# Kernel optimization log

Hardware: AMD Instinct MI355X
Metric: run time of the kernel (lower is better)

## Reference

```python
import math
import jax, jax.numpy as jnp
import numpy as np

D_EMBD = 1024
N_HEAD = 16
BLOCK = 2048
B, T = 4, 2048


def setup_inputs() -> dict:
    key = jax.random.key(0)
    ks = jax.random.split(key, 5)
    d = D_EMBD
    return {
        "x": jax.random.normal(ks[0], (B, T, d), dtype=jnp.float32),
        "Wq": jax.random.normal(ks[1], (d, d), dtype=jnp.float32),
        "bq": jnp.zeros((d,), dtype=jnp.float32),
        "Wk": jax.random.normal(ks[2], (d, d), dtype=jnp.float32),
        "bk": jnp.zeros((d,), dtype=jnp.float32),
        "Wv": jax.random.normal(ks[3], (d, d), dtype=jnp.float32),
        "bv": jnp.zeros((d,), dtype=jnp.float32),
        "Wp": jax.random.normal(ks[4], (d, d), dtype=jnp.float32),
        "bp": jnp.zeros((d,), dtype=jnp.float32),
    }


def reference(x, Wq, bq, Wk, bk, Wv, bv, Wp, bp):
    Bb, Tt, C = x.shape
    n_head = N_HEAD
    hd = C // n_head  # head dim
    # QKV projections -> [B, H, T, hd]
    def split_heads(y):
        return y.reshape(Bb, Tt, n_head, hd).transpose(0, 2, 1, 3)
    Q = split_heads(x @ Wq + bq)
    K = split_heads(x @ Wk + bk)
    V = split_heads(x @ Wv + bv)
    # scores [B, H, T, T]
    attn = jnp.einsum('bhqd,bhkd->bhqk', Q, K) / math.sqrt(hd)
    # causal mask: -inf strictly above diagonal (matches triu(ones*-inf, 1))
    causal = jnp.tril(jnp.ones((Tt, Tt), dtype=bool))
    attn = jnp.where(causal, attn, -jnp.inf)
    attn = jax.nn.softmax(attn, axis=-1)
    y = jnp.einsum('bhqk,bhkd->bhqd', attn, V)
    y = y.transpose(0, 2, 1, 3).reshape(Bb, Tt, C)
    return y @ Wp + bp
```

## Files before the change

kernel.cpp:

```cpp
#include <hip/hip_runtime.h>
#include <stdint.h>
#include <stddef.h>

#define TT 2048
#define CC 1024
#define BBATCH 4
#define HH 16
#define HD 64
#define MTOT (BBATCH * TT)

typedef __bf16 bf16_t;
typedef __bf16 bf16x4 __attribute__((ext_vector_type(4)));
typedef __bf16 bf16x8 __attribute__((ext_vector_type(8)));
typedef float f32x4 __attribute__((ext_vector_type(4)));
typedef float f32x16 __attribute__((ext_vector_type(16)));

typedef const __attribute__((address_space(1))) uint32_t* as1_u32p;
typedef __attribute__((address_space(3))) uint32_t* as3_u32p;

__device__ __forceinline__ f32x4 mfma16(bf16x8 a, bf16x8 b, f32x4 c) {
  return __builtin_amdgcn_mfma_f32_16x16x32_bf16(a, b, c, 0, 0, 0);
}
__device__ __forceinline__ f32x16 mfma32(bf16x8 a, bf16x8 b, f32x16 c) {
  return __builtin_amdgcn_mfma_f32_32x32x16_bf16(a, b, c, 0, 0, 0);
}

__device__ __forceinline__ void gload_lds16(void* lds, const void* g) {
  __builtin_amdgcn_global_load_lds((as1_u32p)g, (as3_u32p)lds, 16, 0, 0);
}

__device__ __forceinline__ bf16x8 rd32(const char* t, int row, int lane) {
  int sl = (lane >> 4) ^ ((row >> 1) & 3);
  return *(const bf16x8*)(t + row * 64 + sl * 16);
}
__device__ __forceinline__ bf16x8 rd32r(const char* t, int row, int slot) {
  return *(const bf16x8*)(t + row * 128 + ((slot ^ (row & 7)) * 16));
}

__global__ void split_x_kernel(const float* __restrict__ x, bf16_t* __restrict__ xh,
                               bf16_t* __restrict__ xl, int n4) {
  int stride = gridDim.x * blockDim.x;
  for (int i = blockIdx.x * blockDim.x + threadIdx.x; i < n4; i += stride) {
    float4 v = ((const float4*)x)[i];
    float vv[4] = {v.x, v.y, v.z, v.w};
    bf16x4 hv, lv;
#pragma unroll
    for (int j = 0; j < 4; ++j) {
      bf16_t h = (bf16_t)vv[j];
      hv[j] = h;
      lv[j] = (bf16_t)(vv[j] - (float)h);
    }
    *(bf16x4*)(xh + (size_t)i * 4) = hv;
    *(bf16x4*)(xl + (size_t)i * 4) = lv;
  }
}

__global__ void transpose_split_kernel(const float* __restrict__ Wq, const float* __restrict__ Wk,
                                       const float* __restrict__ Wv, const float* __restrict__ Wp,
                                       bf16_t* __restrict__ wqkh, bf16_t* __restrict__ wqkl,
                                       bf16_t* __restrict__ wv_t, bf16_t* __restrict__ wp_t) {
  __shared__ float tile[32][33];
  int mat = blockIdx.z;
  const float* W = (mat == 0) ? Wq : (mat == 1) ? Wk : (mat == 2) ? Wv : Wp;
  int tx = threadIdx.x, ty = threadIdx.y;
  int n0 = blockIdx.x * 32, k0 = blockIdx.y * 32;
#pragma unroll
  for (int j = 0; j < 32; j += 8)
    tile[ty + j][tx] = W[(size_t)(k0 + ty + j) * CC + n0 + tx];
  __syncthreads();
#pragma unroll
  for (int j = 0; j < 32; j += 8) {
    float v = tile[tx][ty + j];
    int n = n0 + ty + j, k = k0 + tx;
    if (mat <= 1) {
      bf16_t h = (bf16_t)v;
      size_t o = (size_t)(mat * CC + n) * CC + k;
      wqkh[o] = h;
      wqkl[o] = (bf16_t)(v - (float)h);
    } else {
      bf16_t* dst = (mat == 2) ? wv_t : wp_t;
      dst[(size_t)n * CC + k] = (bf16_t)v;
    }
  }
}

__global__ __launch_bounds__(512, 2) void gemm_qk_kernel(
    const bf16_t* __restrict__ Ah, const bf16_t* __restrict__ Al,
    const bf16_t* __restrict__ Bh, const bf16_t* __restrict__ Bl,
    const float* __restrict__ bq, const float* __restrict__ bk,
    bf16_t* __restrict__ qh, bf16_t* __restrict__ ql,
    bf16_t* __restrict__ kh, bf16_t* __restrict__ kl) {
  __shared__ __align__(16) char s_ah[2][16384];
  __shared__ __align__(16) char s_al[2][16384];
  __shared__ __align__(16) char s_bh[2][16384];
  __shared__ __align__(16) char s_bl[2][16384];

  const int blk = blockIdx.x;
  const int bn = blk & 7;
  const int bm = blk >> 3;
  const int tid = threadIdx.x, w = tid >> 6, lane = tid & 63;
  const int wr = w >> 2, wc = w & 3;
  const int qi = lane & 15, hi = lane >> 4;

  const int c0 = w * 2, c1 = w * 2 + 1;
  const int srow0 = c0 * 16 + (lane >> 2);
  const int srow1 = c1 * 16 + (lane >> 2);
  const int ssl0 = (lane & 3) ^ ((srow0 >> 1) & 3);
  const int ssl1 = (lane & 3) ^ ((srow1 >> 1) & 3);
  const size_t a_off0 = (size_t)(bm * 256 + srow0) * CC + ssl0 * 8;
  const size_t a_off1 = (size_t)(bm * 256 + srow1) * CC + ssl1 * 8;
  const size_t b_off0 = (size_t)(bn * 256 + srow0) * CC + ssl0 * 8;
  const size_t b_off1 = (size_t)(bn * 256 + srow1) * CC + ssl1 * 8;

  f32x4 acc[8][4] = {};

#define STAGE_QK(buf, k0)                                        \
  do {                                                           \
    gload_lds16(s_ah[buf] + c0 * 1024, Ah + a_off0 + (k0));      \
    gload_lds16(s_ah[buf] + c1 * 1024, Ah + a_off1 + (k0));      \
    gload_lds16(s_al[buf] + c0 * 1024, Al + a_off0 + (k0));      \
    gload_lds16(s_al[buf] + c1 * 1024, Al + a_off1 + (k0));      \
    gload_lds16(s_bh[buf] + c0 * 1024, Bh + b_off0 + (k0));      \
    gload_lds16(s_bh[buf] + c1 * 1024, Bh + b_off1 + (k0));      \
    gload_lds16(s_bl[buf] + c0 * 1024, Bl + b_off0 + (k0));      \
    gload_lds16(s_bl[buf] + c1 * 1024, Bl + b_off1 + (k0));      \
  } while (0)

  STAGE_QK(0, 0);
  int cur = 0;
  for (int ks = 0; ks < 32; ++ks) {
    if (ks < 31) {
      STAGE_QK(cur ^ 1, (ks + 1) * 32);
      asm volatile("s_waitcnt vmcnt(8)" ::: "memory");
    } else {
      asm volatile("s_waitcnt vmcnt(0)" ::: "memory");
    }
    __builtin_amdgcn_s_barrier();

    bf16x8 bfh[4], bfl[4];
#pragma unroll
    for (int ni = 0; ni < 4; ++ni) {
      int br = wc * 64 + ni * 16 + qi;
      bfh[ni] = rd32(s_bh[cur], br, lane);
      bfl[ni] = rd32(s_bl[cur], br, lane);
    }
    __builtin_amdgcn_s_setprio(1);
#pragma unroll
    for (int mi = 0; mi < 8; ++mi) {
      int ar = wr * 128 + mi * 16 + qi;
      bf16x8 ahf = rd32(s_ah[cur], ar, lane);
      bf16x8 alf = rd32(s_al[cur], ar, lane);
#pragma unroll
      for (int ni = 0; ni < 4; ++ni) {
        acc[mi][ni] = mfma16(ahf, bfh[ni], acc[mi][ni]);
        acc[mi][ni] = mfma16(ahf, bfl[ni], acc[mi][ni]);
        acc[mi][ni] = mfma16(alf, bfh[ni], acc[mi][ni]);
      }
    }
    __builtin_amdgcn_s_setprio(0);
    asm volatile("s_waitcnt lgkmcnt(0)" ::: "memory");
    __builtin_amdgcn_s_barrier();
    cur ^= 1;
  }
#undef STAGE_QK

  const int which = bn >> 2;
  const float* bias = which ? bk : bq;
  bf16_t* oh = which ? kh : qh;
  bf16_t* ol = which ? kl : ql;
#pragma unroll
  for (int mi = 0; mi < 8; ++mi) {
#pragma unroll
    for (int ni = 0; ni < 4; ++ni) {
      const int col = bn * 256 + wc * 64 + ni * 16 + qi;
      const int c1i = col & 1023;
      const int h = c1i >> 6, d = c1i & 63;
#pragma unroll
      for (int r = 0; r < 4; ++r) {
        const int row = bm * 256 + wr * 128 + mi * 16 + hi * 4 + r;
        const int b = row >> 11, t = row & 2047;
        float v = acc[mi][ni][r] + bias[c1i];
        if (!which) v *= 0.125f;
        const size_t off = ((size_t)(b * HH + h) * TT + t) * HD + d;
        bf16_t hv = (bf16_t)v;
        oh[off] = hv;
        ol[off] = (bf16_t)(v - (float)hv);
      }
    }
  }
}

template <int MODE>
__global__ __launch_bounds__(256) void gemm_kernel(
    const bf16_t* __restrict__ Ah,
    const bf16_t* __restrict__ Bh,
    const float* __restrict__ bias0,
    void* __restrict__ out0) {
  __shared__ __align__(16) char smem[2 * 8192];
  char* sAh = smem;
  char* sBh = smem + 8192;

  const int bn = blockIdx.x, bm = blockIdx.y;
  const int tid = threadIdx.x, w = tid >> 6, lane = tid & 63;
  const int wr = w >> 1, wc = w & 1;

  f32x4 acc[4][4] = {};

  for (int ks = 0; ks < 32; ++ks) {
    const int k0 = ks * 32;
    __syncthreads();
#pragma unroll
    for (int it = 0; it < 2; ++it) {
      int c = it * 4 + w;
      int row = c * 16 + (lane >> 2);
      int sl = (lane & 3) ^ ((row >> 1) & 3);
      size_t aoff = (size_t)(bm * 128 + row) * CC + k0 + sl * 8;
      size_t boff = (size_t)(bn * 128 + row) * CC + k0 + sl * 8;
      gload_lds16(sAh + c * 1024, Ah + aoff);
      gload_lds16(sBh + c * 1024, Bh + boff);
    }
    __syncthreads();

    bf16x8 afh[4], bfh[4];
#pragma unroll
    for (int i = 0; i < 4; ++i) {
      int ar = wr * 64 + i * 16 + (lane & 15);
      int br = wc * 64 + i * 16 + (lane & 15);
      afh[i] = rd32(sAh, ar, lane);
      bfh[i] = rd32(sBh, br, lane);
    }
#pragma unroll
    for (int mi = 0; mi < 4; ++mi) {
#pragma unroll
      for (int ni = 0; ni < 4; ++ni) {
        acc[mi][ni] = mfma16(afh[mi], bfh[ni], acc[mi][ni]);
      }
    }
  }

#pragma unroll
  for (int mi = 0; mi < 4; ++mi) {
#pragma unroll
    for (int ni = 0; ni < 4; ++ni) {
      const int col = bn * 128 + wc * 64 + ni * 16 + (lane & 15);
#pragma unroll
      for (int r = 0; r < 4; ++r) {
        const int row = bm * 128 + wr * 64 + mi * 16 + (lane >> 4) * 4 + r;
        float v = acc[mi][ni][r];
        if (MODE == 1) {
          const int h = col >> 6, d = col & 63;
          const int b = row >> 11, t = row & 2047;
          float vv = v + bias0[col];
          ((bf16_t*)out0)[((size_t)(b * HH + h) * HD + d) * TT + t] = (bf16_t)vv;
        } else {
          ((float*)out0)[(size_t)row * CC + col] = v + bias0[col];
        }
      }
    }
  }
}

__global__ __launch_bounds__(512, 1) void attn_kernel(
    const bf16_t* __restrict__ qh, const bf16_t* __restrict__ ql,
    const bf16_t* __restrict__ kh, const bf16_t* __restrict__ kl,
    const bf16_t* __restrict__ vt, bf16_t* __restrict__ y) {
  __shared__ __align__(16) char s_kh[2][8192];
  __shared__ __align__(16) char s_kl[2][8192];
  __shared__ __align__(16) char s_vt[2][8192];

  const int blk = blockIdx.x;
  const int qb = (int)((0x12560347u >> ((blk >> 6) * 4)) & 7u);
  const int bh = (blk & 7) * 8 + ((blk >> 3) & 7);
  const int b = bh >> 4, h = bh & 15;
  const int tid = threadIdx.x, w = tid >> 6, lane = tid & 63;
  const int l31 = lane & 31, hi = lane >> 5;

  const int strow = w * 8 + (lane >> 3);
  const int sl = (lane & 7) ^ (strow & 7);
  const int ksrow = (strow & ~12) | ((strow & 4) << 1) | ((strow & 8) >> 1);
  const size_t koff = ((size_t)bh * TT + ksrow) * HD + sl * 8;
  const size_t voff = ((size_t)bh * HD + strow) * TT + sl * 8;
  const int ch = w * 1024;

#define STAGE_ATTN(buf, kt)                                            \
  do {                                                                 \
    gload_lds16(s_kh[buf] + ch, kh + koff + (size_t)(kt) * 64 * HD);   \
    gload_lds16(s_kl[buf] + ch, kl + koff + (size_t)(kt) * 64 * HD);   \
    gload_lds16(s_vt[buf] + ch, vt + voff + (size_t)(kt) * 64);        \
  } while (0)

  const int ktmax = 4 * qb + 3;
  const int qrow0 = qb * 256 + w * 32;
  const int qv = qrow0 + l31;

  bf16x8 qhf[4], qlf[4];
#pragma unroll
  for (int kc = 0; kc < 4; ++kc) {
    size_t off = ((size_t)bh * TT + qv) * HD + kc * 16 + hi * 8;
    qhf[kc] = *(const bf16x8*)(qh + off);
    qlf[kc] = *(const bf16x8*)(ql + off);
  }

  f32x16 o0 = {}, o1 = {};
  float m = -1e30f, l = 0.f;

  STAGE_ATTN(0, 0);
  int cur = 0;
  for (int kt = 0; kt <= ktmax; ++kt) {
    if (kt < ktmax) {
      STAGE_ATTN(cur ^ 1, kt + 1);
      asm volatile("s_waitcnt vmcnt(3)" ::: "memory");
    } else {
      asm volatile("s_waitcnt vmcnt(0)" ::: "memory");
    }
    __builtin_amdgcn_s_barrier();

    const char* ckh = s_kh[cur];
    const char* ckl = s_kl[cur];
    const char* cvt = s_vt[cur];
    const bool active = (qrow0 + 31 >= kt * 64);
    if (active) {
      f32x16 s0 = {}, s1 = {};
#pragma unroll
      for (int kc = 0; kc < 4; ++kc) {
        bf16x8 kfh = rd32r(ckh, l31, kc * 2 + hi);
        bf16x8 kfl = rd32r(ckl, l31, kc * 2 + hi);
        s0 = mfma32(kfh, qhf[kc], s0);
        s0 = mfma32(kfl, qhf[kc], s0);
        s0 = mfma32(kfh, qlf[kc], s0);
      }
#pragma unroll
      for (int kc = 0; kc < 4; ++kc) {
        bf16x8 kfh = rd32r(ckh, 32 + l31, kc * 2 + hi);
        bf16x8 kfl = rd32r(ckl, 32 + l31, kc * 2 + hi);
        s1 = mfma32(kfh, qhf[kc], s1);
        s1 = mfma32(kfl, qhf[kc], s1);
        s1 = mfma32(kfh, qlf[kc], s1);
      }

      if (kt * 64 + 63 > qrow0) {
#pragma unroll
        for (int r = 0; r < 16; ++r) {
          const int kvb = kt * 64 + (r & 7) + 8 * hi + 16 * (r >> 3);
          if (kvb > qv) s0[r] = -1e30f;
          if (kvb + 32 > qv) s1[r] = -1e30f;
        }
      }

      float t8[8];
#pragma unroll
      for (int r = 0; r < 8; ++r)
        t8[r] = fmaxf(fmaxf(s0[r], s0[r + 8]), fmaxf(s1[r], s1[r + 8]));
      float t4a = fmaxf(t8[0], t8[4]), t4b = fmaxf(t8[1], t8[5]);
      float t4c = fmaxf(t8[2], t8[6]), t4d = fmaxf(t8[3], t8[7]);
      float tmax = fmaxf(fmaxf(t4a, t4b), fmaxf(t4c, t4d));
      tmax = fmaxf(tmax, __shfl_xor(tmax, 32));

      const float mnew = fmaxf(m, tmax);
      if (!__all(tmax <= m)) {
        const float sc = __expf(m - mnew);
        l *= sc;
#pragma unroll
        for (int r = 0; r < 16; ++r) { o0[r] *= sc; o1[r] *= sc; }
        m = mnew;
      }

#pragma unroll
      for (int r = 0; r < 16; ++r) {
        s0[r] = __expf(s0[r] - m);
        s1[r] = __expf(s1[r] - m);
      }
      float p8[8];
#pragma unroll
      for (int r = 0; r < 8; ++r)
        p8[r] = (s0[r] + s0[r + 8]) + (s1[r] + s1[r + 8]);
      float ps = ((p8[0] + p8[1]) + (p8[2] + p8[3])) + ((p8[4] + p8[5]) + (p8[6] + p8[7]));
      ps += __shfl_xor(ps, 32);
      l += ps;

      bf16x8 pa[4];
#pragma unroll
      for (int cc = 0; cc < 4; ++cc) {
#pragma unroll
        for (int j = 0; j < 8; ++j)
          pa[cc][j] = (bf16_t)((cc >> 1) ? s1[8 * (cc & 1) + j] : s0[8 * (cc & 1) + j]);
      }

#pragma unroll
      for (int cc = 0; cc < 4; ++cc) {
        bf16x8 vf0 = rd32r(cvt, l31, cc * 2 + hi);
        bf16x8 vf1 = rd32r(cvt, 32 + l31, cc * 2 + hi);
        o0 = mfma32(vf0, pa[cc], o0);
        o1 = mfma32(vf1, pa[cc], o1);
      }
    }

    asm volatile("s_waitcnt lgkmcnt(0)" ::: "memory");
    __builtin_amdgcn_s_barrier();
    cur ^= 1;
  }

  const float inv = 1.f / l;
  bf16_t* yb = y + (size_t)(b * TT + qv) * CC + h * HD;
#pragma unroll
  for (int g = 0; g < 4; ++g) {
    bf16x4 ov0, ov1;
#pragma unroll
    for (int r = 0; r < 4; ++r) {
      ov0[r] = (bf16_t)(o0[g * 4 + r] * inv);
      ov1[r] = (bf16_t)(o1[g * 4 + r] * inv);
    }
    *(bf16x4*)(yb + g * 8 + hi * 4) = ov0;
    *(bf16x4*)(yb + 32 + g * 8 + hi * 4) = ov1;
  }
#undef STAGE_ATTN
}

extern "C" void kernel_launch(void* const* d_in, const int* in_sizes, int n_in,
                              void* d_out, int out_size, void* d_ws, size_t ws_size,
                              hipStream_t stream) {
  (void)in_sizes; (void)n_in; (void)out_size; (void)ws_size;
  const float* x  = (const float*)d_in[0];
  const float* Wq = (const float*)d_in[1];
  const float* bq = (const float*)d_in[2];
  const float* Wk = (const float*)d_in[3];
  const float* bk = (const float*)d_in[4];
  const float* Wv = (const float*)d_in[5];
  const float* bv = (const float*)d_in[6];
  const float* Wp = (const float*)d_in[7];
  const float* bp = (const float*)d_in[8];

  char* ws = (char*)d_ws;
  const size_t MB = 1024 * 1024;
  bf16_t* xh   = (bf16_t*)(ws + 0 * MB);
  bf16_t* xl   = (bf16_t*)(ws + 16 * MB);
  bf16_t* wqkh = (bf16_t*)(ws + 32 * MB);
  bf16_t* wqkl = (bf16_t*)(ws + 36 * MB);
  bf16_t* wv_t = (bf16_t*)(ws + 40 * MB);
  bf16_t* wp_t = (bf16_t*)(ws + 42 * MB);
  bf16_t* qhw  = (bf16_t*)(ws + 44 * MB);
  bf16_t* qlw  = (bf16_t*)(ws + 60 * MB);
  bf16_t* khw  = (bf16_t*)(ws + 76 * MB);
  bf16_t* klw  = (bf16_t*)(ws + 92 * MB);
  bf16_t* vtw  = (bf16_t*)(ws + 108 * MB);
  bf16_t* yw   = (bf16_t*)(ws + 124 * MB);

  split_x_kernel<<<2048, 256, 0, stream>>>(x, xh, xl, MTOT * CC / 4);
  transpose_split_kernel<<<dim3(32, 32, 4), dim3(32, 8), 0, stream>>>(
      Wq, Wk, Wv, Wp, wqkh, wqkl, wv_t, wp_t);
  gemm_qk_kernel<<<256, 512, 0, stream>>>(
      xh, xl, wqkh, wqkl, bq, bk, qhw, qlw, khw, klw);
  gemm_kernel<1><<<dim3(8, 64), 256, 0, stream>>>(
      xh, wv_t, bv, vtw);
  attn_kernel<<<512, 512, 0, stream>>>(qhw, qlw, khw, klw, vtw, yw);
  gemm_kernel<2><<<dim3(8, 64), 256, 0, stream>>>(
      yw, wp_t, bp, d_out);
}
```

Before: 264.6 us.

## Load K/V tiles directly into registers in attention, drop LDS staging

The attention kernel stops staging K, K-low and V^T tiles through double-buffered shared memory. Each wave now reads its own K and V fragments straight from global memory into registers and prefetches the next K tile one iteration ahead. Block size drops from 512 to 256 threads (128 query rows) with 1024 blocks, launch bounds allowing 2 blocks per CU, and the query-block order becomes simple descending. This removes LDS traffic and most barriers, but every wave now fetches K/V itself with no sharing across waves, which raises global/L2 traffic and register pressure.

```diff
diff --git a/kernel.cpp b/kernel.cpp
--- a/kernel.cpp
+++ b/kernel.cpp
@@ -32,9 +32,6 @@
 __device__ __forceinline__ bf16x8 rd32(const char* t, int row, int lane) {
   int sl = (lane >> 4) ^ ((row >> 1) & 3);
   return *(const bf16x8*)(t + row * 64 + sl * 16);
-}
-__device__ __forceinline__ bf16x8 rd32r(const char* t, int row, int slot) {
-  return *(const bf16x8*)(t + row * 128 + ((slot ^ (row & 7)) * 16));
 }
 
 __global__ void split_x_kernel(const float* __restrict__ x, bf16_t* __restrict__ xh,
@@ -260,38 +257,25 @@
   }
 }
 
-__global__ __launch_bounds__(512, 1) void attn_kernel(
+__global__ __launch_bounds__(256, 2) void attn_kernel(
     const bf16_t* __restrict__ qh, const bf16_t* __restrict__ ql,
     const bf16_t* __restrict__ kh, const bf16_t* __restrict__ kl,
     const bf16_t* __restrict__ vt, bf16_t* __restrict__ y) {
-  __shared__ __align__(16) char s_kh[2][8192];
-  __shared__ __align__(16) char s_kl[2][8192];
-  __shared__ __align__(16) char s_vt[2][8192];
-
   const int blk = blockIdx.x;
-  const int qb = (int)((0x12560347u >> ((blk >> 6) * 4)) & 7u);
+  const int qb = 15 - (blk >> 6);
   const int bh = (blk & 7) * 8 + ((blk >> 3) & 7);
   const int b = bh >> 4, h = bh & 15;
   const int tid = threadIdx.x, w = tid >> 6, lane = tid & 63;
   const int l31 = lane & 31, hi = lane >> 5;
 
-  const int strow = w * 8 + (lane >> 3);
-  const int sl = (lane & 7) ^ (strow & 7);
-  const int ksrow = (strow & ~12) | ((strow & 4) << 1) | ((strow & 8) >> 1);
-  const size_t koff = ((size_t)bh * TT + ksrow) * HD + sl * 8;
-  const size_t voff = ((size_t)bh * HD + strow) * TT + sl * 8;
-  const int ch = w * 1024;
-
-#define STAGE_ATTN(buf, kt)                                            \
-  do {                                                                 \
-    gload_lds16(s_kh[buf] + ch, kh + koff + (size_t)(kt) * 64 * HD);   \
-    gload_lds16(s_kl[buf] + ch, kl + koff + (size_t)(kt) * 64 * HD);   \
-    gload_lds16(s_vt[buf] + ch, vt + voff + (size_t)(kt) * 64);        \
-  } while (0)
-
-  const int ktmax = 4 * qb + 3;
-  const int qrow0 = qb * 256 + w * 32;
+  const int ktmax = 2 * qb + 1;
+  const int qrow0 = qb * 128 + w * 32;
   const int qv = qrow0 + l31;
+
+  const int kr = (l31 & ~12) | ((l31 & 4) << 1) | ((l31 & 8) >> 1);
+  const bf16_t* khp = kh + ((size_t)bh * TT + kr) * HD + hi * 8;
+  const bf16_t* klp = kl + ((size_t)bh * TT + kr) * HD + hi * 8;
+  const bf16_t* vtp = vt + ((size_t)bh * HD + l31) * TT + hi * 8;
 
   bf16x8 qhf[4], qlf[4];
 #pragma unroll
@@ -304,38 +288,47 @@
   f32x16 o0 = {}, o1 = {};
   float m = -1e30f, l = 0.f;
 
-  STAGE_ATTN(0, 0);
-  int cur = 0;
+  bf16x8 k0h[4], k0l[4], k1h[4], k1l[4];
+#pragma unroll
+  for (int kc = 0; kc < 4; ++kc) {
+    k0h[kc] = *(const bf16x8*)(khp + kc * 16);
+    k1h[kc] = *(const bf16x8*)(khp + 32 * HD + kc * 16);
+    k0l[kc] = *(const bf16x8*)(klp + kc * 16);
+    k1l[kc] = *(const bf16x8*)(klp + 32 * HD + kc * 16);
+  }
+
   for (int kt = 0; kt <= ktmax; ++kt) {
-    if (kt < ktmax) {
-      STAGE_ATTN(cur ^ 1, kt + 1);
-      asm volatile("s_waitcnt vmcnt(3)" ::: "memory");
-    } else {
-      asm volatile("s_waitcnt vmcnt(0)" ::: "memory");
-    }
     __builtin_amdgcn_s_barrier();
-
-    const char* ckh = s_kh[cur];
-    const char* ckl = s_kl[cur];
-    const char* cvt = s_vt[cur];
     const bool active = (qrow0 + 31 >= kt * 64);
     if (active) {
       f32x16 s0 = {}, s1 = {};
 #pragma unroll
       for (int kc = 0; kc < 4; ++kc) {
-        bf16x8 kfh = rd32r(ckh, l31, kc * 2 + hi);
-        bf16x8 kfl = rd32r(ckl, l31, kc * 2 + hi);
-        s0 = mfma32(kfh, qhf[kc], s0);
-        s0 = mfma32(kfl, qhf[kc], s0);
-        s0 = mfma32(kfh, qlf[kc], s0);
-      }
-#pragma unroll
-      for (int kc = 0; kc < 4; ++kc) {
-        bf16x8 kfh = rd32r(ckh, 32 + l31, kc * 2 + hi);
-        bf16x8 kfl = rd32r(ckl, 32 + l31, kc * 2 + hi);
-        s1 = mfma32(kfh, qhf[kc], s1);
-        s1 = mfma32(kfl, qhf[kc], s1);
-        s1 = mfma32(kfh, qlf[kc], s1);
+        s0 = mfma32(k0h[kc], qhf[kc], s0);
+        s0 = mfma32(k0l[kc], qhf[kc], s0);
+        s0 = mfma32(k0h[kc], qlf[kc], s0);
+        s1 = mfma32(k1h[kc], qhf[kc], s1);
+        s1 = mfma32(k1l[kc], qhf[kc], s1);
+        s1 = mfma32(k1h[kc], qlf[kc], s1);
+      }
+
+      bf16x8 v0[4], v1[4];
+      const bf16_t* vp = vtp + (size_t)kt * 64;
+#pragma unroll
+      for (int cc = 0; cc < 4; ++cc) {
+        v0[cc] = *(const bf16x8*)(vp + cc * 16);
+        v1[cc] = *(const bf16x8*)(vp + 32 * TT + cc * 16);
+      }
+      if (kt < ktmax && qrow0 + 31 >= (kt + 1) * 64) {
+        const bf16_t* kp = khp + (size_t)(kt + 1) * 64 * HD;
+        const bf16_t* kp2 = klp + (size_t)(kt + 1) * 64 * HD;
+#pragma unroll
+        for (int kc = 0; kc < 4; ++kc) {
+          k0h[kc] = *(const bf16x8*)(kp + kc * 16);
+          k1h[kc] = *(const bf16x8*)(kp + 32 * HD + kc * 16);
+          k0l[kc] = *(const bf16x8*)(kp2 + kc * 16);
+          k1l[kc] = *(const bf16x8*)(kp2 + 32 * HD + kc * 16);
+        }
       }
 
       if (kt * 64 + 63 > qrow0) {
@@ -388,16 +381,10 @@
 
 #pragma unroll
       for (int cc = 0; cc < 4; ++cc) {
-        bf16x8 vf0 = rd32r(cvt, l31, cc * 2 + hi);
-        bf16x8 vf1 = rd32r(cvt, 32 + l31, cc * 2 + hi);
-        o0 = mfma32(vf0, pa[cc], o0);
-        o1 = mfma32(vf1, pa[cc], o1);
-      }
-    }
-
-    asm volatile("s_waitcnt lgkmcnt(0)" ::: "memory");
-    __builtin_amdgcn_s_barrier();
-    cur ^= 1;
+        o0 = mfma32(v0[cc], pa[cc], o0);
+        o1 = mfma32(v1[cc], pa[cc], o1);
+      }
+    }
   }
 
   const float inv = 1.f / l;
@@ -413,7 +400,6 @@
     *(bf16x4*)(yb + g * 8 + hi * 4) = ov0;
     *(bf16x4*)(yb + 32 + g * 8 + hi * 4) = ov1;
   }
-#undef STAGE_ATTN
 }
 
 extern "C" void kernel_launch(void* const* d_in, const int* in_sizes, int n_in,
@@ -452,7 +438,7 @@
       xh, xl, wqkh, wqkl, bq, bk, qhw, qlw, khw, klw);
   gemm_kernel<1><<<dim3(8, 64), 256, 0, stream>>>(
       xh, wv_t, bv, vtw);
-  attn_kernel<<<512, 512, 0, stream>>>(qhw, qlw, khw, klw, vtw, yw);
+  attn_kernel<<<1024, 256, 0, stream>>>(qhw, qlw, khw, klw, vtw, yw);
   gemm_kernel<2><<<dim3(8, 64), 256, 0, stream>>>(
       yw, wp_t, bp, d_out);
 }
```

Result: slower. 357.8 us (+35.2%).
